# Optimization experiments

Measured on AMD Instinct MI355X. Metric: run time of the kernel, lower is better.

Reference implementation:

```python
import jax, jax.numpy as jnp
import numpy as np

N_NODES = 100000
N_EDGES = 1600000
IN_C, HID_C, OUT_C = 128, 128, 64


def setup_inputs() -> dict:
    key = jax.random.key(0)
    k = jax.random.split(key, 5)
    x = jax.random.normal(k[0], (N_NODES, IN_C), dtype=jnp.float32)
    edge_index = jax.random.randint(k[1], (2, N_EDGES), 0, N_NODES, dtype=jnp.int32)
    # Glorot-ish scaling for the GCNConv linear weights
    W1 = jax.random.normal(k[2], (IN_C, HID_C), dtype=jnp.float32) * (1.0 / np.sqrt(IN_C))
    b1 = jnp.zeros((HID_C,), dtype=jnp.float32)
    W2 = jax.random.normal(k[3], (HID_C, OUT_C), dtype=jnp.float32) * (1.0 / np.sqrt(HID_C))
    b2 = jnp.zeros((OUT_C,), dtype=jnp.float32)
    return {"x": x, "edge_index": edge_index, "W1": W1, "b1": b1, "W2": W2, "b2": b2}


def _gcn_conv(h, W, b, src, dst, deg_inv_sqrt, n):
    # h: [N, F_in] -> linear transform, then deg-normalized scatter-add over edges
    h = h @ W  # [N, F_out]
    norm = deg_inv_sqrt[src] * deg_inv_sqrt[dst]  # [E+N] (self-loops included)
    msgs = h[src] * norm[:, None]  # gather + scale
    out = jax.ops.segment_sum(msgs, dst, num_segments=n)  # scatter-add to dst
    return out + b


def reference(x, edge_index, W1, b1, W2, b2):
    n = x.shape[0]
    loops = jnp.arange(n, dtype=edge_index.dtype)
    src = jnp.concatenate([edge_index[0], loops])  # add self-loops (PyG default)
    dst = jnp.concatenate([edge_index[1], loops])
    deg = jax.ops.segment_sum(jnp.ones_like(dst, dtype=x.dtype), dst, num_segments=n)
    deg_inv_sqrt = jax.lax.rsqrt(deg)  # deg >= 1 due to self-loops

    h = _gcn_conv(x, W1, b1, src, dst, deg_inv_sqrt, n)
    h = jax.nn.relu(h)
    # F.dropout(training=False) is identity at inference
    h = _gcn_conv(h, W2, b2, src, dst, deg_inv_sqrt, n)
    return jax.nn.log_softmax(h, axis=1)
```

## Files before the change

kernel.cpp:

```cpp
#include <hip/hip_runtime.h>
#include <hip/hip_bf16.h>


typedef unsigned short ushortT;
typedef unsigned char ucharT;
typedef __attribute__((ext_vector_type(8))) short short8v;
typedef __attribute__((ext_vector_type(4))) float float4v;
typedef __attribute__((ext_vector_type(2))) float float2v;
typedef __attribute__((ext_vector_type(8))) unsigned short ushort8v;

__device__ __forceinline__ float bf2f(ushortT u) {
  union { unsigned int i; float f; } x;
  x.i = ((unsigned int)u) << 16;
  return x.f;
}

__device__ __forceinline__ ushortT f2bf(float f) {
  __hip_bfloat16 h = __float2bfloat16(f);
  return *(ushortT*)&h;
}

__device__ __forceinline__ ucharT f2fp8(float f) {
  unsigned int w = __builtin_amdgcn_cvt_pk_fp8_f32(f, f, 0, false);
  return (ucharT)(w & 0xff);
}

__device__ __forceinline__ void fp8x8_to_f32(unsigned int lo, unsigned int hi,
                                             float* f) {
  float2v p0 = __builtin_amdgcn_cvt_pk_f32_fp8(lo, false);
  float2v p1 = __builtin_amdgcn_cvt_pk_f32_fp8(lo, true);
  float2v p2 = __builtin_amdgcn_cvt_pk_f32_fp8(hi, false);
  float2v p3 = __builtin_amdgcn_cvt_pk_f32_fp8(hi, true);
  f[0] = p0[0]; f[1] = p0[1]; f[2] = p1[0]; f[3] = p1[1];
  f[4] = p2[0]; f[5] = p2[1]; f[6] = p3[0]; f[7] = p3[1];
}

__device__ __forceinline__ void fp8x4_to_f32(unsigned int w, float* f) {
  float2v p0 = __builtin_amdgcn_cvt_pk_f32_fp8(w, false);
  float2v p1 = __builtin_amdgcn_cvt_pk_f32_fp8(w, true);
  f[0] = p0[0]; f[1] = p0[1]; f[2] = p1[0]; f[3] = p1[1];
}

__device__ __forceinline__ bool probe_isbf(const void* xv) {
  const ushortT* xr = (const ushortT*)xv;
  const int lane = threadIdx.x & 63;
  float v = bf2f(xr[lane]);
  bool sane = isfinite(v) && fabsf(v) < 1e4f;
  return __ballot(sane) == ~0ull;
}

__global__ __launch_bounds__(256) void wprep_k(const void* __restrict__ W1v,
                                               const void* __restrict__ W2v,
                                               const void* __restrict__ xv,
                                               ushortT* __restrict__ Wt1,
                                               ushortT* __restrict__ Wt2) {
  const bool isbf = probe_isbf(xv);
  const int i = blockIdx.x * 256 + threadIdx.x;
  if (i < 16384) {
    int nn = i & 127, k = i >> 7;
    ushortT v = isbf ? ((const ushortT*)W1v)[k * 128 + nn]
                     : f2bf(((const float*)W1v)[k * 128 + nn]);
    Wt1[nn * 128 + k] = v;
  } else if (i < 24576) {
    int j = i - 16384;
    int nn = j & 63, k = j >> 6;
    ushortT v = isbf ? ((const ushortT*)W2v)[k * 64 + nn]
                     : f2bf(((const float*)W2v)[k * 64 + nn]);
    Wt2[nn * 128 + k] = v;
  }
}


__global__ __launch_bounds__(256) void bhist_k(const int* __restrict__ dst, int E, int B,
                                               int* __restrict__ gbc) {
  __shared__ int h[512];
  const int tid = threadIdx.x;
  for (int i = tid; i < B; i += 256) h[i] = 0;
  __syncthreads();
  const int i0 = blockIdx.x * 8192;
  const int iend = min(i0 + 8192, E);
  for (int i = i0 + tid; i < iend; i += 256) atomicAdd(&h[dst[i] >> 8], 1);
  __syncthreads();
  for (int i = tid; i < B; i += 256)
    if (h[i]) atomicAdd(&gbc[i], h[i]);
}

__global__ __launch_bounds__(256) void bscan_k(const int* __restrict__ gbc, int B,
                                               int* __restrict__ bbase,
                                               int* __restrict__ gcur) {
  __shared__ int p[256];
  const int t = threadIdx.x;
  int a = (2 * t < B) ? gbc[2 * t] : 0;
  int b = (2 * t + 1 < B) ? gbc[2 * t + 1] : 0;
  const int sum = a + b;
  p[t] = sum;
  __syncthreads();
  int run = sum;
  for (int off = 1; off < 256; off <<= 1) {
    int v = (t >= off) ? p[t - off] : 0;
    __syncthreads();
    run += v;
    p[t] = run;
    __syncthreads();
  }
  const int excl = run - sum;
  if (2 * t < B) { bbase[2 * t] = excl; gcur[2 * t] = excl; }
  if (2 * t + 1 < B) { bbase[2 * t + 1] = excl + a; gcur[2 * t + 1] = excl + a; }
}

__global__ __launch_bounds__(256) void bin_k(const int* __restrict__ srcv,
                                             const int* __restrict__ dstv, int E, int B,
                                             int* __restrict__ gcur,
                                             int* __restrict__ tmp) {
  __shared__ int hist[512];
  __shared__ int base[512];
  const int tid = threadIdx.x;
  const int i0 = blockIdx.x * 8192;
  const int iend = min(i0 + 8192, E);
  for (int i = tid; i < B; i += 256) hist[i] = 0;
  __syncthreads();
  for (int i = i0 + tid; i < iend; i += 256) atomicAdd(&hist[dstv[i] >> 8], 1);
  __syncthreads();
  for (int i = tid; i < B; i += 256) {
    int h = hist[i];
    base[i] = h ? atomicAdd(&gcur[i], h) : 0;
    hist[i] = 0;
  }
  __syncthreads();
  for (int i = i0 + tid; i < iend; i += 256) {
    int d = dstv[i];
    int s = srcv[i];
    int b = d >> 8;
    int l = atomicAdd(&hist[b], 1);
    tmp[base[b] + l] = s | ((d & 255) << 17);
  }
}

__global__ __launch_bounds__(256) void csr_k(const int* __restrict__ tmp,
                                             const int* __restrict__ bbase,
                                             const int* __restrict__ gbc, int n,
                                             int2* __restrict__ rpc,
                                             float* __restrict__ dis,
                                             int* __restrict__ col) {
  __shared__ int lhist[256];
  __shared__ int lexcl[256];
  const int b = blockIdx.x;
  const int tid = threadIdx.x;
  const int e0 = bbase[b];
  const int e1 = e0 + gbc[b];
  lhist[tid] = 0;
  __syncthreads();
  for (int i = e0 + tid; i < e1; i += 256) atomicAdd(&lhist[tmp[i] >> 17], 1);
  __syncthreads();
  const int v = lhist[tid];
  int run = v;
  lexcl[tid] = run;
  __syncthreads();
  for (int off = 1; off < 256; off <<= 1) {
    int t = (tid >= off) ? lexcl[tid - off] : 0;
    __syncthreads();
    run += t;
    lexcl[tid] = run;
    __syncthreads();
  }
  const int excl = run - v;
  const int node = (b << 8) + tid;
  if (node < n) {
    rpc[node] = make_int2(e0 + excl, v);
    dis[node] = rsqrtf((float)(v + 1));
  }
  lhist[tid] = 0;
  lexcl[tid] = excl;
  __syncthreads();
  for (int i = e0 + tid; i < e1; i += 256) {
    int p = tmp[i];
    int dloc = p >> 17;
    int s = p & 131071;
    int l = atomicAdd(&lhist[dloc], 1);
    col[e0 + lexcl[dloc] + l] = s;
  }
}

__global__ __launch_bounds__(512) void gemm1_k(const void* __restrict__ xv,
                                               const ushortT* __restrict__ Wt1,
                                               const float* __restrict__ dis,
                                               ucharT* __restrict__ Hb8, int n) {
  __shared__ ushortT sW[128 * 132];
  const bool isbf = probe_isbf(xv);
  const int tid = threadIdx.x;
  for (int i = tid; i < 4096; i += 512) {
    int nn = i >> 5, k4 = (i & 31) * 4;
    *(ushort4*)&sW[nn * 132 + k4] = *(const ushort4*)&Wt1[nn * 128 + k4];
  }
  __syncthreads();

  const int wave = tid >> 6;
  const int lane = tid & 63;
  const int m = lane & 15;
  const int quad = lane >> 4;
  const int row = blockIdx.x * 128 + wave * 16 + m;
  const int rowc = min(row, n - 1);

  float4v acc[8];
#pragma unroll
  for (int t = 0; t < 8; ++t) acc[t] = (float4v)(0.f);

  if (isbf) {
    const ushortT* xp = (const ushortT*)xv + (size_t)rowc * 128 + quad * 8;
#pragma unroll
    for (int kc = 0; kc < 4; ++kc) {
      short8v af = *(const short8v*)(xp + kc * 32);
#pragma unroll
      for (int nb = 0; nb < 8; ++nb) {
        short8v bf = *(const short8v*)&sW[(nb * 16 + m) * 132 + kc * 32 + quad * 8];
        acc[nb] = __builtin_amdgcn_mfma_f32_16x16x32_bf16(af, bf, acc[nb], 0, 0, 0);
      }
    }
  } else {
    const float* xp = (const float*)xv + (size_t)rowc * 128 + quad * 8;
#pragma unroll
    for (int kc = 0; kc < 4; ++kc) {
      float4 lo = *(const float4*)(xp + kc * 32);
      float4 hi = *(const float4*)(xp + kc * 32 + 4);
      short8v af;
      af[0] = (short)f2bf(lo.x); af[1] = (short)f2bf(lo.y);
      af[2] = (short)f2bf(lo.z); af[3] = (short)f2bf(lo.w);
      af[4] = (short)f2bf(hi.x); af[5] = (short)f2bf(hi.y);
      af[6] = (short)f2bf(hi.z); af[7] = (short)f2bf(hi.w);
#pragma unroll
      for (int nb = 0; nb < 8; ++nb) {
        short8v bf = *(const short8v*)&sW[(nb * 16 + m) * 132 + kc * 32 + quad * 8];
        acc[nb] = __builtin_amdgcn_mfma_f32_16x16x32_bf16(af, bf, acc[nb], 0, 0, 0);
      }
    }
  }

#pragma unroll
  for (int r = 0; r < 4; ++r) {
    int grow = blockIdx.x * 128 + wave * 16 + quad * 4 + r;
    if (grow <= n) {
      float sc = (grow < n) ? dis[grow] : 0.f;
#pragma unroll
      for (int nb = 0; nb < 8; ++nb)
        Hb8[(size_t)grow * 128 + nb * 16 + m] =
            (grow < n) ? f2fp8(sc * acc[nb][r]) : (ucharT)0;
    }
  }
}

__global__ __launch_bounds__(256) void agg1_k(const ucharT* __restrict__ Hb8,
                                              const int* __restrict__ col,
                                              const int2* __restrict__ rpc,
                                              const float* __restrict__ dis,
                                              const void* __restrict__ b1v,
                                              const void* __restrict__ xv,
                                              ushortT* __restrict__ Ab, int n) {
  const bool isbf = probe_isbf(xv);
  const int tid = threadIdx.x;
  const int lane = tid & 63;
  const int wave = tid >> 6;
  const int quad = lane >> 4;
  const int m = lane & 15;
  const int c8 = m * 8;
  const int node = blockIdx.x * 16 + wave * 4 + quad;
  const bool valid = node < n;
  const int nd = valid ? node : (n - 1);

  const int2 rc = rpc[nd];
  const int start = rc.x;
  const int cnt = valid ? rc.y : 0;
  const float din = dis[nd];

  const uint2 hsp = *(const uint2*)&Hb8[((unsigned)(valid ? node : n) << 7) + (unsigned)c8];
  float b[8];
  if (isbf) {
    ushort8v bb = *(const ushort8v*)((const ushortT*)b1v + c8);
#pragma unroll
    for (int k = 0; k < 8; ++k) b[k] = bf2f(bb[k]);
  } else {
    const float* bf = (const float*)b1v + c8;
#pragma unroll
    for (int k = 0; k < 8; ++k) b[k] = bf[k];
  }

  int cmax = cnt;
  cmax = max(cmax, __shfl_xor(cmax, 16));
  cmax = max(cmax, __shfl_xor(cmax, 32));
  const int cmaxs = __builtin_amdgcn_readfirstlane(cmax);

  float2v acc[4];
#pragma unroll
  for (int k = 0; k < 4; ++k) acc[k] = (float2v)(0.f);

  for (int e = 0; e < cmaxs; e += 4) {
#pragma unroll
    for (int u = 0; u < 4; ++u) {
      const int ee = e + u;
      int s = col[start + ee];
      s = (ee < cnt) ? s : n;
      const uint2 h = *(const uint2*)&Hb8[((unsigned)s << 7) + (unsigned)c8];
      acc[0] += __builtin_amdgcn_cvt_pk_f32_fp8(h.x, false);
      acc[1] += __builtin_amdgcn_cvt_pk_f32_fp8(h.x, true);
      acc[2] += __builtin_amdgcn_cvt_pk_f32_fp8(h.y, false);
      acc[3] += __builtin_amdgcn_cvt_pk_f32_fp8(h.y, true);
    }
  }

  if (valid) {
    float hs[8];
    fp8x8_to_f32(hsp.x, hsp.y, hs);
    ushort8v o;
#pragma unroll
    for (int k = 0; k < 4; ++k) {
      o[2 * k]     = f2bf(fmaxf(fmaf(din, acc[k][0] + hs[2 * k],     b[2 * k]),     0.f));
      o[2 * k + 1] = f2bf(fmaxf(fmaf(din, acc[k][1] + hs[2 * k + 1], b[2 * k + 1]), 0.f));
    }
    *(ushort8v*)&Ab[(size_t)node * 128 + c8] = o;
  }
}

__global__ __launch_bounds__(512) void gemm2_k(const ushortT* __restrict__ Ab,
                                               const ushortT* __restrict__ Wt2,
                                               const float* __restrict__ dis,
                                               ucharT* __restrict__ H2b8, int n) {
  __shared__ ushortT sW[64 * 132];
  const int tid = threadIdx.x;
  for (int i = tid; i < 2048; i += 512) {
    int nn = i >> 5, k4 = (i & 31) * 4;
    *(ushort4*)&sW[nn * 132 + k4] = *(const ushort4*)&Wt2[nn * 128 + k4];
  }
  __syncthreads();

  const int wave = tid >> 6;
  const int lane = tid & 63;
  const int m = lane & 15;
  const int quad = lane >> 4;
  const int row = blockIdx.x * 128 + wave * 16 + m;
  const int rowc = min(row, n - 1);

  float4v acc[4];
#pragma unroll
  for (int t = 0; t < 4; ++t) acc[t] = (float4v)(0.f);

  const ushortT* ap = Ab + (size_t)rowc * 128 + quad * 8;
#pragma unroll
  for (int kc = 0; kc < 4; ++kc) {
    short8v af = *(const short8v*)(ap + kc * 32);
#pragma unroll
    for (int nb = 0; nb < 4; ++nb) {
      short8v bf = *(const short8v*)&sW[(nb * 16 + m) * 132 + kc * 32 + quad * 8];
      acc[nb] = __builtin_amdgcn_mfma_f32_16x16x32_bf16(af, bf, acc[nb], 0, 0, 0);
    }
  }

#pragma unroll
  for (int r = 0; r < 4; ++r) {
    int grow = blockIdx.x * 128 + wave * 16 + quad * 4 + r;
    if (grow <= n) {
      float sc = (grow < n) ? dis[grow] : 0.f;
#pragma unroll
      for (int nb = 0; nb < 4; ++nb)
        H2b8[(size_t)grow * 64 + nb * 16 + m] =
            (grow < n) ? f2fp8(sc * acc[nb][r]) : (ucharT)0;
    }
  }
}

__global__ __launch_bounds__(256) void agg2_k(const ucharT* __restrict__ H2b8,
                                              const int* __restrict__ col,
                                              const int2* __restrict__ rpc,
                                              const float* __restrict__ dis,
                                              const void* __restrict__ b2v,
                                              const void* __restrict__ xv,
                                              void* __restrict__ outv, int n) {
  const bool isbf = probe_isbf(xv);
  const int tid = threadIdx.x;
  const int lane = tid & 63;
  const int wave = tid >> 6;
  const int quad = lane >> 4;
  const int m = lane & 15;
  const int c4 = m * 4;
  const int node = blockIdx.x * 16 + wave * 4 + quad;
  const bool valid = node < n;
  const int nd = valid ? node : (n - 1);

  const int2 rc = rpc[nd];
  const int start = rc.x;
  const int cnt = valid ? rc.y : 0;
  const float din = dis[nd];

  const unsigned int hsp =
      *(const unsigned int*)&H2b8[((unsigned)(valid ? node : n) << 6) + (unsigned)c4];
  float b[4];
  if (isbf) {
    ushort4 bb = *(const ushort4*)((const ushortT*)b2v + c4);
    b[0] = bf2f(bb.x); b[1] = bf2f(bb.y); b[2] = bf2f(bb.z); b[3] = bf2f(bb.w);
  } else {
    const float* bf = (const float*)b2v + c4;
#pragma unroll
    for (int k = 0; k < 4; ++k) b[k] = bf[k];
  }

  int cmax = cnt;
  cmax = max(cmax, __shfl_xor(cmax, 16));
  cmax = max(cmax, __shfl_xor(cmax, 32));
  const int cmaxs = __builtin_amdgcn_readfirstlane(cmax);

  float2v acc[2];
  acc[0] = (float2v)(0.f);
  acc[1] = (float2v)(0.f);

  for (int e = 0; e < cmaxs; e += 4) {
#pragma unroll
    for (int u = 0; u < 4; ++u) {
      const int ee = e + u;
      int s = col[start + ee];
      s = (ee < cnt) ? s : n;
      const unsigned int h = *(const unsigned int*)&H2b8[((unsigned)s << 6) + (unsigned)c4];
      acc[0] += __builtin_amdgcn_cvt_pk_f32_fp8(h, false);
      acc[1] += __builtin_amdgcn_cvt_pk_f32_fp8(h, true);
    }
  }

  float hs[4];
  fp8x4_to_f32(hsp, hs);
  float v[4];
  v[0] = fmaf(din, acc[0][0] + hs[0], b[0]);
  v[1] = fmaf(din, acc[0][1] + hs[1], b[1]);
  v[2] = fmaf(din, acc[1][0] + hs[2], b[2]);
  v[3] = fmaf(din, acc[1][1] + hs[3], b[3]);

  float mx = fmaxf(fmaxf(v[0], v[1]), fmaxf(v[2], v[3]));
  for (int off = 1; off < 16; off <<= 1) mx = fmaxf(mx, __shfl_xor(mx, off));
  float ssum = __expf(v[0] - mx) + __expf(v[1] - mx) + __expf(v[2] - mx) + __expf(v[3] - mx);
  for (int off = 1; off < 16; off <<= 1) ssum += __shfl_xor(ssum, off);
  const float lse = mx + __logf(ssum);

  if (valid) {
    if (isbf) {
      ushort4 o;
      o.x = f2bf(v[0] - lse); o.y = f2bf(v[1] - lse);
      o.z = f2bf(v[2] - lse); o.w = f2bf(v[3] - lse);
      *(ushort4*)((__hip_bfloat16*)outv + (size_t)node * 64 + c4) = o;
    } else {
      float4 o = make_float4(v[0] - lse, v[1] - lse, v[2] - lse, v[3] - lse);
      *(float4*)((float*)outv + (size_t)node * 64 + c4) = o;
    }
  }
}


extern "C" void kernel_launch(void* const* d_in, const int* in_sizes, int n_in,
                              void* d_out, int out_size, void* d_ws, size_t ws_size,
                              hipStream_t stream) {
  const void* x  = d_in[0];
  const int*  ei = (const int*)d_in[1];
  const void* W1 = d_in[2];
  const void* b1 = d_in[3];
  const void* W2 = d_in[4];
  const void* b2 = d_in[5];

  const int n = in_sizes[0] / 128;
  const int E = in_sizes[1] / 2;
  const int B = (n + 255) >> 8;
  const int* srcv = ei;
  const int* dstv = ei + E;

  char* p = (char*)d_ws;
  auto alloc = [&](size_t bytes) {
    char* q = p;
    p += (bytes + 255) & ~(size_t)255;
    return q;
  };
  ucharT* Hb8 = (ucharT*)alloc((size_t)(n + 1) * 128);
  ucharT* H2b8 = (ucharT*)alloc((size_t)(n + 1) * 64);
  ushortT* Ab = (ushortT*)alloc((size_t)n * 128 * 2);
  float* dis = (float*)alloc((size_t)n * 4);
  int2* rpc = (int2*)alloc((size_t)n * 8);
  int* gbc = (int*)alloc(512 * 4);
  int* bbase = (int*)alloc(512 * 4);
  int* gcur = (int*)alloc(512 * 4);
  ushortT* Wt1 = (ushortT*)alloc(16384 * 2);
  ushortT* Wt2 = (ushortT*)alloc(8192 * 2);
  int* tmp = (int*)alloc((size_t)E * 4);
  int* col = (int*)alloc(((size_t)E + 4096) * 4);

  (void)hipMemsetAsync(gbc, 0, 512 * sizeof(int), stream);

  const int gChunks = (E + 8191) / 8192;

  wprep_k<<<96, 256, 0, stream>>>(W1, W2, x, Wt1, Wt2);
  bhist_k<<<gChunks, 256, 0, stream>>>(dstv, E, B, gbc);
  bscan_k<<<1, 256, 0, stream>>>(gbc, B, bbase, gcur);
  bin_k<<<gChunks, 256, 0, stream>>>(srcv, dstv, E, B, gcur, tmp);
  csr_k<<<B, 256, 0, stream>>>(tmp, bbase, gbc, n, rpc, dis, col);

  gemm1_k<<<(n + 128) / 128, 512, 0, stream>>>(x, Wt1, dis, Hb8, n);
  agg1_k<<<(n + 15) / 16, 256, 0, stream>>>(Hb8, col, rpc, dis, b1, x, Ab, n);
  gemm2_k<<<(n + 128) / 128, 512, 0, stream>>>(Ab, Wt2, dis, H2b8, n);
  agg2_k<<<(n + 15) / 16, 256, 0, stream>>>(H2b8, col, rpc, dis, b2, x, d_out, n);
}
```

Before: 238.4 us.

## Fuse CSR build into cooperative kernel and fuse layer-1 aggregation with GEMM2

Replaces the memset and five graph-preprocessing launches with one cooperative kernel on 256 blocks that uses grid-wide syncs between the histogram, scan, binning and CSR phases. It also fuses the layer-1 aggregation with the second GEMM: each 512-thread block aggregates 128 rows into shared memory as bf16 and runs the MFMA directly from there, dropping the Ab round trip through global memory. The costs are fewer aggregation blocks in flight, each with more serial work (four sub-rows per wave), and preprocessing limited to a fixed grid of 256 blocks.

```diff
diff --git a/kernel.cpp b/kernel.cpp
--- a/kernel.cpp
+++ b/kernel.cpp
@@ -1,5 +1,8 @@
 #include <hip/hip_runtime.h>
 #include <hip/hip_bf16.h>
+#include <hip/hip_cooperative_groups.h>
+
+namespace cg = cooperative_groups;
 
 
 typedef unsigned short ushortT;
@@ -49,135 +52,140 @@
   return __ballot(sane) == ~0ull;
 }
 
-__global__ __launch_bounds__(256) void wprep_k(const void* __restrict__ W1v,
+__global__ __launch_bounds__(256) void build_k(const int* __restrict__ srcv,
+                                               const int* __restrict__ dstv,
+                                               int E, int B, int n,
+                                               const void* __restrict__ W1v,
                                                const void* __restrict__ W2v,
                                                const void* __restrict__ xv,
                                                ushortT* __restrict__ Wt1,
-                                               ushortT* __restrict__ Wt2) {
+                                               ushortT* __restrict__ Wt2,
+                                               int* __restrict__ gbc,
+                                               int* __restrict__ bbase,
+                                               int* __restrict__ gcur,
+                                               int* __restrict__ tmp,
+                                               int2* __restrict__ rpc,
+                                               float* __restrict__ dis,
+                                               int* __restrict__ col) {
+  cg::grid_group grid = cg::this_grid();
+  __shared__ int sh0[512];
+  __shared__ int sh1[512];
+  const int tid = threadIdx.x;
+  const int gid = blockIdx.x * 256 + tid;
+  const int gsz = gridDim.x * 256;
   const bool isbf = probe_isbf(xv);
-  const int i = blockIdx.x * 256 + threadIdx.x;
-  if (i < 16384) {
-    int nn = i & 127, k = i >> 7;
-    ushortT v = isbf ? ((const ushortT*)W1v)[k * 128 + nn]
-                     : f2bf(((const float*)W1v)[k * 128 + nn]);
-    Wt1[nn * 128 + k] = v;
-  } else if (i < 24576) {
-    int j = i - 16384;
-    int nn = j & 63, k = j >> 6;
-    ushortT v = isbf ? ((const ushortT*)W2v)[k * 64 + nn]
-                     : f2bf(((const float*)W2v)[k * 64 + nn]);
-    Wt2[nn * 128 + k] = v;
-  }
-}
-
-
-__global__ __launch_bounds__(256) void bhist_k(const int* __restrict__ dst, int E, int B,
-                                               int* __restrict__ gbc) {
-  __shared__ int h[512];
-  const int tid = threadIdx.x;
-  for (int i = tid; i < B; i += 256) h[i] = 0;
-  __syncthreads();
-  const int i0 = blockIdx.x * 8192;
-  const int iend = min(i0 + 8192, E);
-  for (int i = i0 + tid; i < iend; i += 256) atomicAdd(&h[dst[i] >> 8], 1);
-  __syncthreads();
-  for (int i = tid; i < B; i += 256)
-    if (h[i]) atomicAdd(&gbc[i], h[i]);
-}
-
-__global__ __launch_bounds__(256) void bscan_k(const int* __restrict__ gbc, int B,
-                                               int* __restrict__ bbase,
-                                               int* __restrict__ gcur) {
-  __shared__ int p[256];
-  const int t = threadIdx.x;
-  int a = (2 * t < B) ? gbc[2 * t] : 0;
-  int b = (2 * t + 1 < B) ? gbc[2 * t + 1] : 0;
-  const int sum = a + b;
-  p[t] = sum;
-  __syncthreads();
-  int run = sum;
-  for (int off = 1; off < 256; off <<= 1) {
-    int v = (t >= off) ? p[t - off] : 0;
-    __syncthreads();
-    run += v;
-    p[t] = run;
-    __syncthreads();
-  }
-  const int excl = run - sum;
-  if (2 * t < B) { bbase[2 * t] = excl; gcur[2 * t] = excl; }
-  if (2 * t + 1 < B) { bbase[2 * t + 1] = excl + a; gcur[2 * t + 1] = excl + a; }
-}
-
-__global__ __launch_bounds__(256) void bin_k(const int* __restrict__ srcv,
-                                             const int* __restrict__ dstv, int E, int B,
-                                             int* __restrict__ gcur,
-                                             int* __restrict__ tmp) {
-  __shared__ int hist[512];
-  __shared__ int base[512];
-  const int tid = threadIdx.x;
-  const int i0 = blockIdx.x * 8192;
-  const int iend = min(i0 + 8192, E);
-  for (int i = tid; i < B; i += 256) hist[i] = 0;
-  __syncthreads();
-  for (int i = i0 + tid; i < iend; i += 256) atomicAdd(&hist[dstv[i] >> 8], 1);
-  __syncthreads();
-  for (int i = tid; i < B; i += 256) {
-    int h = hist[i];
-    base[i] = h ? atomicAdd(&gcur[i], h) : 0;
-    hist[i] = 0;
-  }
-  __syncthreads();
-  for (int i = i0 + tid; i < iend; i += 256) {
-    int d = dstv[i];
-    int s = srcv[i];
-    int b = d >> 8;
-    int l = atomicAdd(&hist[b], 1);
-    tmp[base[b] + l] = s | ((d & 255) << 17);
-  }
-}
-
-__global__ __launch_bounds__(256) void csr_k(const int* __restrict__ tmp,
-                                             const int* __restrict__ bbase,
-                                             const int* __restrict__ gbc, int n,
-                                             int2* __restrict__ rpc,
-                                             float* __restrict__ dis,
-                                             int* __restrict__ col) {
-  __shared__ int lhist[256];
-  __shared__ int lexcl[256];
-  const int b = blockIdx.x;
-  const int tid = threadIdx.x;
-  const int e0 = bbase[b];
-  const int e1 = e0 + gbc[b];
-  lhist[tid] = 0;
-  __syncthreads();
-  for (int i = e0 + tid; i < e1; i += 256) atomicAdd(&lhist[tmp[i] >> 17], 1);
-  __syncthreads();
-  const int v = lhist[tid];
-  int run = v;
-  lexcl[tid] = run;
-  __syncthreads();
-  for (int off = 1; off < 256; off <<= 1) {
-    int t = (tid >= off) ? lexcl[tid - off] : 0;
-    __syncthreads();
-    run += t;
-    lexcl[tid] = run;
-    __syncthreads();
-  }
-  const int excl = run - v;
-  const int node = (b << 8) + tid;
-  if (node < n) {
-    rpc[node] = make_int2(e0 + excl, v);
-    dis[node] = rsqrtf((float)(v + 1));
-  }
-  lhist[tid] = 0;
-  lexcl[tid] = excl;
-  __syncthreads();
-  for (int i = e0 + tid; i < e1; i += 256) {
-    int p = tmp[i];
-    int dloc = p >> 17;
-    int s = p & 131071;
-    int l = atomicAdd(&lhist[dloc], 1);
-    col[e0 + lexcl[dloc] + l] = s;
+  const int nChunks = (E + 8191) / 8192;
+
+  for (int i = gid; i < 512; i += gsz) gbc[i] = 0;
+  for (int i = gid; i < 24576; i += gsz) {
+    if (i < 16384) {
+      int nn = i & 127, k = i >> 7;
+      ushortT v = isbf ? ((const ushortT*)W1v)[k * 128 + nn]
+                       : f2bf(((const float*)W1v)[k * 128 + nn]);
+      Wt1[nn * 128 + k] = v;
+    } else {
+      int j = i - 16384;
+      int nn = j & 63, k = j >> 6;
+      ushortT v = isbf ? ((const ushortT*)W2v)[k * 64 + nn]
+                       : f2bf(((const float*)W2v)[k * 64 + nn]);
+      Wt2[nn * 128 + k] = v;
+    }
+  }
+  grid.sync();
+
+  for (int c = blockIdx.x; c < nChunks; c += gridDim.x) {
+    for (int i = tid; i < B; i += 256) sh0[i] = 0;
+    __syncthreads();
+    const int i0 = c * 8192;
+    const int iend = min(i0 + 8192, E);
+    for (int i = i0 + tid; i < iend; i += 256) atomicAdd(&sh0[dstv[i] >> 8], 1);
+    __syncthreads();
+    for (int i = tid; i < B; i += 256)
+      if (sh0[i]) atomicAdd(&gbc[i], sh0[i]);
+    __syncthreads();
+  }
+  grid.sync();
+
+  if (blockIdx.x == 0) {
+    const int t = tid;
+    int a = (2 * t < B) ? gbc[2 * t] : 0;
+    int b = (2 * t + 1 < B) ? gbc[2 * t + 1] : 0;
+    const int sum = a + b;
+    sh0[t] = sum;
+    __syncthreads();
+    int run = sum;
+    for (int off = 1; off < 256; off <<= 1) {
+      int v = (t >= off) ? sh0[t - off] : 0;
+      __syncthreads();
+      run += v;
+      sh0[t] = run;
+      __syncthreads();
+    }
+    const int excl = run - sum;
+    if (2 * t < B) { bbase[2 * t] = excl; gcur[2 * t] = excl; }
+    if (2 * t + 1 < B) { bbase[2 * t + 1] = excl + a; gcur[2 * t + 1] = excl + a; }
+  }
+  grid.sync();
+
+  for (int c = blockIdx.x; c < nChunks; c += gridDim.x) {
+    const int i0 = c * 8192;
+    const int iend = min(i0 + 8192, E);
+    for (int i = tid; i < B; i += 256) sh0[i] = 0;
+    __syncthreads();
+    for (int i = i0 + tid; i < iend; i += 256) atomicAdd(&sh0[dstv[i] >> 8], 1);
+    __syncthreads();
+    for (int i = tid; i < B; i += 256) {
+      int h = sh0[i];
+      sh1[i] = h ? atomicAdd(&gcur[i], h) : 0;
+      sh0[i] = 0;
+    }
+    __syncthreads();
+    for (int i = i0 + tid; i < iend; i += 256) {
+      int d = dstv[i];
+      int s = srcv[i];
+      int b = d >> 8;
+      int l = atomicAdd(&sh0[b], 1);
+      tmp[sh1[b] + l] = s | ((d & 255) << 17);
+    }
+    __syncthreads();
+  }
+  grid.sync();
+
+  for (int b = blockIdx.x; b < B; b += gridDim.x) {
+    const int e0 = bbase[b];
+    const int e1 = e0 + gbc[b];
+    sh0[tid] = 0;
+    __syncthreads();
+    for (int i = e0 + tid; i < e1; i += 256) atomicAdd(&sh0[tmp[i] >> 17], 1);
+    __syncthreads();
+    const int v = sh0[tid];
+    int run = v;
+    sh1[tid] = run;
+    __syncthreads();
+    for (int off = 1; off < 256; off <<= 1) {
+      int t = (tid >= off) ? sh1[tid - off] : 0;
+      __syncthreads();
+      run += t;
+      sh1[tid] = run;
+      __syncthreads();
+    }
+    const int excl = run - v;
+    const int node = (b << 8) + tid;
+    if (node < n) {
+      rpc[node] = make_int2(e0 + excl, v);
+      dis[node] = rsqrtf((float)(v + 1));
+    }
+    sh0[tid] = 0;
+    sh1[tid] = excl;
+    __syncthreads();
+    for (int i = e0 + tid; i < e1; i += 256) {
+      int p = tmp[i];
+      int dloc = p >> 17;
+      int s = p & 131071;
+      int l = atomicAdd(&sh0[dloc], 1);
+      col[e0 + sh1[dloc] + l] = s;
+    }
+    __syncthreads();
   }
 }
 
@@ -248,30 +256,30 @@
   }
 }
 
-__global__ __launch_bounds__(256) void agg1_k(const ucharT* __restrict__ Hb8,
-                                              const int* __restrict__ col,
-                                              const int2* __restrict__ rpc,
-                                              const float* __restrict__ dis,
-                                              const void* __restrict__ b1v,
-                                              const void* __restrict__ xv,
-                                              ushortT* __restrict__ Ab, int n) {
+__global__ __launch_bounds__(512) void mid_k(const ucharT* __restrict__ Hb8,
+                                             const int* __restrict__ col,
+                                             const int2* __restrict__ rpc,
+                                             const float* __restrict__ dis,
+                                             const void* __restrict__ b1v,
+                                             const ushortT* __restrict__ Wt2,
+                                             const void* __restrict__ xv,
+                                             ucharT* __restrict__ H2b8, int n) {
+  __shared__ ushortT sA[128 * 132];
+  __shared__ ushortT sW[64 * 132];
   const bool isbf = probe_isbf(xv);
   const int tid = threadIdx.x;
+  for (int i = tid; i < 2048; i += 512) {
+    int nn = i >> 5, k4 = (i & 31) * 4;
+    *(ushort4*)&sW[nn * 132 + k4] = *(const ushort4*)&Wt2[nn * 128 + k4];
+  }
+
   const int lane = tid & 63;
   const int wave = tid >> 6;
   const int quad = lane >> 4;
   const int m = lane & 15;
   const int c8 = m * 8;
-  const int node = blockIdx.x * 16 + wave * 4 + quad;
-  const bool valid = node < n;
-  const int nd = valid ? node : (n - 1);
-
-  const int2 rc = rpc[nd];
-  const int start = rc.x;
-  const int cnt = valid ? rc.y : 0;
-  const float din = dis[nd];
-
-  const uint2 hsp = *(const uint2*)&Hb8[((unsigned)(valid ? node : n) << 7) + (unsigned)c8];
+  const int node0 = blockIdx.x * 128;
+
   float b[8];
   if (isbf) {
     ushort8v bb = *(const ushort8v*)((const ushortT*)b1v + c8);
@@ -283,69 +291,67 @@
     for (int k = 0; k < 8; ++k) b[k] = bf[k];
   }
 
-  int cmax = cnt;
-  cmax = max(cmax, __shfl_xor(cmax, 16));
-  cmax = max(cmax, __shfl_xor(cmax, 32));
-  const int cmaxs = __builtin_amdgcn_readfirstlane(cmax);
-
-  float2v acc[4];
-#pragma unroll
-  for (int k = 0; k < 4; ++k) acc[k] = (float2v)(0.f);
-
-  for (int e = 0; e < cmaxs; e += 4) {
-#pragma unroll
-    for (int u = 0; u < 4; ++u) {
-      const int ee = e + u;
-      int s = col[start + ee];
-      s = (ee < cnt) ? s : n;
-      const uint2 h = *(const uint2*)&Hb8[((unsigned)s << 7) + (unsigned)c8];
-      acc[0] += __builtin_amdgcn_cvt_pk_f32_fp8(h.x, false);
-      acc[1] += __builtin_amdgcn_cvt_pk_f32_fp8(h.x, true);
-      acc[2] += __builtin_amdgcn_cvt_pk_f32_fp8(h.y, false);
-      acc[3] += __builtin_amdgcn_cvt_pk_f32_fp8(h.y, true);
-    }
-  }
-
-  if (valid) {
-    float hs[8];
-    fp8x8_to_f32(hsp.x, hsp.y, hs);
+#pragma unroll
+  for (int s = 0; s < 4; ++s) {
+    const int lrow = s * 32 + wave * 4 + quad;
+    const int node = node0 + lrow;
+    const bool valid = node < n;
+    const int nd = valid ? node : (n - 1);
+    const int2 rc = rpc[nd];
+    const int start = rc.x;
+    const int cnt = valid ? rc.y : 0;
+    const float din = dis[nd];
+    const uint2 hsp =
+        *(const uint2*)&Hb8[((unsigned)(valid ? node : n) << 7) + (unsigned)c8];
+
+    int cmax = cnt;
+    cmax = max(cmax, __shfl_xor(cmax, 16));
+    cmax = max(cmax, __shfl_xor(cmax, 32));
+    const int cmaxs = __builtin_amdgcn_readfirstlane(cmax);
+
+    float2v acc[4];
+#pragma unroll
+    for (int k = 0; k < 4; ++k) acc[k] = (float2v)(0.f);
+
+    for (int e = 0; e < cmaxs; e += 4) {
+#pragma unroll
+      for (int u = 0; u < 4; ++u) {
+        const int ee = e + u;
+        int sidx = col[start + ee];
+        sidx = (ee < cnt) ? sidx : n;
+        const uint2 h = *(const uint2*)&Hb8[((unsigned)sidx << 7) + (unsigned)c8];
+        acc[0] += __builtin_amdgcn_cvt_pk_f32_fp8(h.x, false);
+        acc[1] += __builtin_amdgcn_cvt_pk_f32_fp8(h.x, true);
+        acc[2] += __builtin_amdgcn_cvt_pk_f32_fp8(h.y, false);
+        acc[3] += __builtin_amdgcn_cvt_pk_f32_fp8(h.y, true);
+      }
+    }
+
     ushort8v o;
-#pragma unroll
-    for (int k = 0; k < 4; ++k) {
-      o[2 * k]     = f2bf(fmaxf(fmaf(din, acc[k][0] + hs[2 * k],     b[2 * k]),     0.f));
-      o[2 * k + 1] = f2bf(fmaxf(fmaf(din, acc[k][1] + hs[2 * k + 1], b[2 * k + 1]), 0.f));
-    }
-    *(ushort8v*)&Ab[(size_t)node * 128 + c8] = o;
-  }
-}
-
-__global__ __launch_bounds__(512) void gemm2_k(const ushortT* __restrict__ Ab,
-                                               const ushortT* __restrict__ Wt2,
-                                               const float* __restrict__ dis,
-                                               ucharT* __restrict__ H2b8, int n) {
-  __shared__ ushortT sW[64 * 132];
-  const int tid = threadIdx.x;
-  for (int i = tid; i < 2048; i += 512) {
-    int nn = i >> 5, k4 = (i & 31) * 4;
-    *(ushort4*)&sW[nn * 132 + k4] = *(const ushort4*)&Wt2[nn * 128 + k4];
+    if (valid) {
+      float hs[8];
+      fp8x8_to_f32(hsp.x, hsp.y, hs);
+#pragma unroll
+      for (int k = 0; k < 4; ++k) {
+        o[2 * k]     = f2bf(fmaxf(fmaf(din, acc[k][0] + hs[2 * k],     b[2 * k]),     0.f));
+        o[2 * k + 1] = f2bf(fmaxf(fmaf(din, acc[k][1] + hs[2 * k + 1], b[2 * k + 1]), 0.f));
+      }
+    } else {
+#pragma unroll
+      for (int k = 0; k < 8; ++k) o[k] = 0;
+    }
+    *(ushort8v*)&sA[lrow * 132 + c8] = o;
   }
   __syncthreads();
 
-  const int wave = tid >> 6;
-  const int lane = tid & 63;
-  const int m = lane & 15;
-  const int quad = lane >> 4;
-  const int row = blockIdx.x * 128 + wave * 16 + m;
-  const int rowc = min(row, n - 1);
-
   float4v acc[4];
 #pragma unroll
   for (int t = 0; t < 4; ++t) acc[t] = (float4v)(0.f);
 
-  const ushortT* ap = Ab + (size_t)rowc * 128 + quad * 8;
+  const int arow = wave * 16 + m;
 #pragma unroll
   for (int kc = 0; kc < 4; ++kc) {
-    short8v af = *(const short8v*)(ap + kc * 32);
+    short8v af = *(const short8v*)&sA[arow * 132 + kc * 32 + quad * 8];
 #pragma unroll
     for (int nb = 0; nb < 4; ++nb) {
       short8v bf = *(const short8v*)&sW[(nb * 16 + m) * 132 + kc * 32 + quad * 8];
@@ -460,9 +466,9 @@
   const void* W2 = d_in[4];
   const void* b2 = d_in[5];
 
-  const int n = in_sizes[0] / 128;
-  const int E = in_sizes[1] / 2;
-  const int B = (n + 255) >> 8;
+  int n = in_sizes[0] / 128;
+  int E = in_sizes[1] / 2;
+  int B = (n + 255) >> 8;
   const int* srcv = ei;
   const int* dstv = ei + E;
 
@@ -474,7 +480,6 @@
   };
   ucharT* Hb8 = (ucharT*)alloc((size_t)(n + 1) * 128);
   ucharT* H2b8 = (ucharT*)alloc((size_t)(n + 1) * 64);
-  ushortT* Ab = (ushortT*)alloc((size_t)n * 128 * 2);
   float* dis = (float*)alloc((size_t)n * 4);
   int2* rpc = (int2*)alloc((size_t)n * 8);
   int* gbc = (int*)alloc(512 * 4);
@@ -485,18 +490,14 @@
   int* tmp = (int*)alloc((size_t)E * 4);
   int* col = (int*)alloc(((size_t)E + 4096) * 4);
 
-  (void)hipMemsetAsync(gbc, 0, 512 * sizeof(int), stream);
-
-  const int gChunks = (E + 8191) / 8192;
-
-  wprep_k<<<96, 256, 0, stream>>>(W1, W2, x, Wt1, Wt2);
-  bhist_k<<<gChunks, 256, 0, stream>>>(dstv, E, B, gbc);
-  bscan_k<<<1, 256, 0, stream>>>(gbc, B, bbase, gcur);
-  bin_k<<<gChunks, 256, 0, stream>>>(srcv, dstv, E, B, gcur, tmp);
-  csr_k<<<B, 256, 0, stream>>>(tmp, bbase, gbc, n, rpc, dis, col);
+  void* bargs[] = {(void*)&srcv, (void*)&dstv, (void*)&E, (void*)&B, (void*)&n,
+                   (void*)&W1, (void*)&W2, (void*)&x, (void*)&Wt1, (void*)&Wt2,
+                   (void*)&gbc, (void*)&bbase, (void*)&gcur, (void*)&tmp,
+                   (void*)&rpc, (void*)&dis, (void*)&col};
+  (void)hipLaunchCooperativeKernel((void*)build_k, dim3(256), dim3(256), bargs,
+                                   0, stream);
 
   gemm1_k<<<(n + 128) / 128, 512, 0, stream>>>(x, Wt1, dis, Hb8, n);
-  agg1_k<<<(n + 15) / 16, 256, 0, stream>>>(Hb8, col, rpc, dis, b1, x, Ab, n);
-  gemm2_k<<<(n + 128) / 128, 512, 0, stream>>>(Ab, Wt2, dis, H2b8, n);
+  mid_k<<<(n + 128) / 128, 512, 0, stream>>>(Hb8, col, rpc, dis, b1, Wt2, x, H2b8, n);
   agg2_k<<<(n + 15) / 16, 256, 0, stream>>>(H2b8, col, rpc, dis, b2, x, d_out, n);
 }
```

After: 370.2 us. 55.3% more time.

## Fuse layer-1 aggregation with layer-2 GEMM through shared memory

Applied to the files above, without the earlier changes.

Merges the first aggregation kernel and the second GEMM into one kernel. Each 512-thread block aggregates 128 nodes into a bf16 tile in LDS and then runs the MFMA GEMM against W2 staged in LDS. This removes the global write and re-read of the intermediate activation matrix and one kernel launch. In exchange, each block uses about 50KB of LDS, which lowers occupancy for the latency-bound gather phase, and the block now holds 4 sequential gather rounds before the GEMM can start.

```diff
diff --git a/kernel.cpp b/kernel.cpp
--- a/kernel.cpp
+++ b/kernel.cpp
@@ -248,30 +248,30 @@
   }
 }
 
-__global__ __launch_bounds__(256) void agg1_k(const ucharT* __restrict__ Hb8,
-                                              const int* __restrict__ col,
-                                              const int2* __restrict__ rpc,
-                                              const float* __restrict__ dis,
-                                              const void* __restrict__ b1v,
-                                              const void* __restrict__ xv,
-                                              ushortT* __restrict__ Ab, int n) {
+__global__ __launch_bounds__(512) void mid_k(const ucharT* __restrict__ Hb8,
+                                             const int* __restrict__ col,
+                                             const int2* __restrict__ rpc,
+                                             const float* __restrict__ dis,
+                                             const void* __restrict__ b1v,
+                                             const ushortT* __restrict__ Wt2,
+                                             const void* __restrict__ xv,
+                                             ucharT* __restrict__ H2b8, int n) {
+  __shared__ ushortT sA[128 * 132];
+  __shared__ ushortT sW[64 * 132];
   const bool isbf = probe_isbf(xv);
   const int tid = threadIdx.x;
+  for (int i = tid; i < 2048; i += 512) {
+    int nn = i >> 5, k4 = (i & 31) * 4;
+    *(ushort4*)&sW[nn * 132 + k4] = *(const ushort4*)&Wt2[nn * 128 + k4];
+  }
+
   const int lane = tid & 63;
   const int wave = tid >> 6;
   const int quad = lane >> 4;
   const int m = lane & 15;
   const int c8 = m * 8;
-  const int node = blockIdx.x * 16 + wave * 4 + quad;
-  const bool valid = node < n;
-  const int nd = valid ? node : (n - 1);
-
-  const int2 rc = rpc[nd];
-  const int start = rc.x;
-  const int cnt = valid ? rc.y : 0;
-  const float din = dis[nd];
-
-  const uint2 hsp = *(const uint2*)&Hb8[((unsigned)(valid ? node : n) << 7) + (unsigned)c8];
+  const int node0 = blockIdx.x * 128;
+
   float b[8];
   if (isbf) {
     ushort8v bb = *(const ushort8v*)((const ushortT*)b1v + c8);
@@ -283,69 +283,67 @@
     for (int k = 0; k < 8; ++k) b[k] = bf[k];
   }
 
-  int cmax = cnt;
-  cmax = max(cmax, __shfl_xor(cmax, 16));
-  cmax = max(cmax, __shfl_xor(cmax, 32));
-  const int cmaxs = __builtin_amdgcn_readfirstlane(cmax);
-
-  float2v acc[4];
-#pragma unroll
-  for (int k = 0; k < 4; ++k) acc[k] = (float2v)(0.f);
-
-  for (int e = 0; e < cmaxs; e += 4) {
-#pragma unroll
-    for (int u = 0; u < 4; ++u) {
-      const int ee = e + u;
-      int s = col[start + ee];
-      s = (ee < cnt) ? s : n;
-      const uint2 h = *(const uint2*)&Hb8[((unsigned)s << 7) + (unsigned)c8];
-      acc[0] += __builtin_amdgcn_cvt_pk_f32_fp8(h.x, false);
-      acc[1] += __builtin_amdgcn_cvt_pk_f32_fp8(h.x, true);
-      acc[2] += __builtin_amdgcn_cvt_pk_f32_fp8(h.y, false);
-      acc[3] += __builtin_amdgcn_cvt_pk_f32_fp8(h.y, true);
-    }
-  }
-
-  if (valid) {
-    float hs[8];
-    fp8x8_to_f32(hsp.x, hsp.y, hs);
+#pragma unroll
+  for (int s = 0; s < 4; ++s) {
+    const int lrow = s * 32 + wave * 4 + quad;
+    const int node = node0 + lrow;
+    const bool valid = node < n;
+    const int nd = valid ? node : (n - 1);
+    const int2 rc = rpc[nd];
+    const int start = rc.x;
+    const int cnt = valid ? rc.y : 0;
+    const float din = dis[nd];
+    const uint2 hsp =
+        *(const uint2*)&Hb8[((unsigned)(valid ? node : n) << 7) + (unsigned)c8];
+
+    int cmax = cnt;
+    cmax = max(cmax, __shfl_xor(cmax, 16));
+    cmax = max(cmax, __shfl_xor(cmax, 32));
+    const int cmaxs = __builtin_amdgcn_readfirstlane(cmax);
+
+    float2v acc[4];
+#pragma unroll
+    for (int k = 0; k < 4; ++k) acc[k] = (float2v)(0.f);
+
+    for (int e = 0; e < cmaxs; e += 4) {
+#pragma unroll
+      for (int u = 0; u < 4; ++u) {
+        const int ee = e + u;
+        int sidx = col[start + ee];
+        sidx = (ee < cnt) ? sidx : n;
+        const uint2 h = *(const uint2*)&Hb8[((unsigned)sidx << 7) + (unsigned)c8];
+        acc[0] += __builtin_amdgcn_cvt_pk_f32_fp8(h.x, false);
+        acc[1] += __builtin_amdgcn_cvt_pk_f32_fp8(h.x, true);
+        acc[2] += __builtin_amdgcn_cvt_pk_f32_fp8(h.y, false);
+        acc[3] += __builtin_amdgcn_cvt_pk_f32_fp8(h.y, true);
+      }
+    }
+
     ushort8v o;
-#pragma unroll
-    for (int k = 0; k < 4; ++k) {
-      o[2 * k]     = f2bf(fmaxf(fmaf(din, acc[k][0] + hs[2 * k],     b[2 * k]),     0.f));
-      o[2 * k + 1] = f2bf(fmaxf(fmaf(din, acc[k][1] + hs[2 * k + 1], b[2 * k + 1]), 0.f));
-    }
-    *(ushort8v*)&Ab[(size_t)node * 128 + c8] = o;
-  }
-}
-
-__global__ __launch_bounds__(512) void gemm2_k(const ushortT* __restrict__ Ab,
-                                               const ushortT* __restrict__ Wt2,
-                                               const float* __restrict__ dis,
-                                               ucharT* __restrict__ H2b8, int n) {
-  __shared__ ushortT sW[64 * 132];
-  const int tid = threadIdx.x;
-  for (int i = tid; i < 2048; i += 512) {
-    int nn = i >> 5, k4 = (i & 31) * 4;
-    *(ushort4*)&sW[nn * 132 + k4] = *(const ushort4*)&Wt2[nn * 128 + k4];
-  }
-  __syncthreads();
-
-  const int wave = tid >> 6;
-  const int lane = tid & 63;
-  const int m = lane & 15;
-  const int quad = lane >> 4;
-  const int row = blockIdx.x * 128 + wave * 16 + m;
-  const int rowc = min(row, n - 1);
+    if (valid) {
+      float hs[8];
+      fp8x8_to_f32(hsp.x, hsp.y, hs);
+#pragma unroll
+      for (int k = 0; k < 4; ++k) {
+        o[2 * k]     = f2bf(fmaxf(fmaf(din, acc[k][0] + hs[2 * k],     b[2 * k]),     0.f));
+        o[2 * k + 1] = f2bf(fmaxf(fmaf(din, acc[k][1] + hs[2 * k + 1], b[2 * k + 1]), 0.f));
+      }
+    } else {
+#pragma unroll
+      for (int k = 0; k < 8; ++k) o[k] = 0;
+    }
+    *(ushort8v*)&sA[lrow * 132 + c8] = o;
+  }
+  __syncthreads();
 
   float4v acc[4];
 #pragma unroll
   for (int t = 0; t < 4; ++t) acc[t] = (float4v)(0.f);
 
-  const ushortT* ap = Ab + (size_t)rowc * 128 + quad * 8;
+  const int arow = wave * 16 + m;
 #pragma unroll
   for (int kc = 0; kc < 4; ++kc) {
-    short8v af = *(const short8v*)(ap + kc * 32);
+    short8v af = *(const short8v*)&sA[arow * 132 + kc * 32 + quad * 8];
 #pragma unroll
     for (int nb = 0; nb < 4; ++nb) {
       short8v bf = *(const short8v*)&sW[(nb * 16 + m) * 132 + kc * 32 + quad * 8];
@@ -474,7 +472,6 @@
   };
   ucharT* Hb8 = (ucharT*)alloc((size_t)(n + 1) * 128);
   ucharT* H2b8 = (ucharT*)alloc((size_t)(n + 1) * 64);
-  ushortT* Ab = (ushortT*)alloc((size_t)n * 128 * 2);
   float* dis = (float*)alloc((size_t)n * 4);
   int2* rpc = (int2*)alloc((size_t)n * 8);
   int* gbc = (int*)alloc(512 * 4);
@@ -496,7 +493,6 @@
   csr_k<<<B, 256, 0, stream>>>(tmp, bbase, gbc, n, rpc, dis, col);
 
   gemm1_k<<<(n + 128) / 128, 512, 0, stream>>>(x, Wt1, dis, Hb8, n);
-  agg1_k<<<(n + 15) / 16, 256, 0, stream>>>(Hb8, col, rpc, dis, b1, x, Ab, n);
-  gemm2_k<<<(n + 128) / 128, 512, 0, stream>>>(Ab, Wt2, dis, H2b8, n);
+  mid_k<<<(n + 128) / 128, 512, 0, stream>>>(Hb8, col, rpc, dis, b1, Wt2, x, H2b8, n);
   agg2_k<<<(n + 15) / 16, 256, 0, stream>>>(H2b8, col, rpc, dis, b2, x, d_out, n);
 }
```

Result: no change. 242.5 us (+1.7%).
